# Kernel tuning notes

Hardware: AMD Instinct MI355X
Metric: run time of the kernel (lower is better)

## Reference

```python
import jax, jax.numpy as jnp
import numpy as np

EPS = 1e-12  # F.normalize eps

def _l2norm(t):
    n = jnp.linalg.norm(t, axis=-1, keepdims=True)
    return t / jnp.maximum(n, EPS)

def setup_inputs() -> dict:
    key = jax.random.key(0)
    ks = jax.random.split(key, 6)
    B, S, H, M = 4, 4096, 1024, 256
    x = jax.random.normal(ks[0], (B, S, H), dtype=jnp.float32)
    W_query = jax.random.normal(ks[1], (M, H), dtype=jnp.float32) * 0.02
    W_key = jax.random.normal(ks[2], (M, H), dtype=jnp.float32) * 0.02
    W_value = jax.random.normal(ks[3], (M, H), dtype=jnp.float32) * 0.02
    W_out = jax.random.normal(ks[4], (H, M), dtype=jnp.float32) * 0.02
    M0 = jnp.zeros((M, M), dtype=jnp.float32)
    return {"x": x, "W_query": W_query, "W_key": W_key, "W_value": W_value,
            "W_out": W_out, "M0": M0, "chunk_size": 64}

def reference(x, W_query, W_key, W_value, W_out, M0, chunk_size):
    B, S, H = x.shape
    Mdim = W_query.shape[0]
    decay, max_m_norm = 0.99, 10.0
    q = jnp.einsum('bsh,mh->bsm', x, W_query)
    k = _l2norm(jnp.einsum('bsh,mh->bsm', x, W_key))
    v = _l2norm(jnp.einsum('bsh,mh->bsm', x, W_value))
    n_chunks = S // chunk_size
    c = chunk_size
    # (n_chunks, B, c, Mdim) so scan iterates over chunks
    qc = q.reshape(B, n_chunks, c, Mdim).transpose(1, 0, 2, 3)
    kc = k.reshape(B, n_chunks, c, Mdim).transpose(1, 0, 2, 3)
    vc = v.reshape(B, n_chunks, c, Mdim).transpose(1, 0, 2, 3)

    def step(Mst, qkv):
        qch, kch, vch = qkv
        # read with state at start of chunk: q @ M.T
        r = jnp.einsum('bcm,nm->bcn', qch, Mst)
        # uniform write, token-level aggregation
        outer = jnp.einsum('bci,bcj->ij', vch, kch) / (B * c)
        Mn = decay * Mst + outer
        nrm = jnp.linalg.norm(Mn)
        Mn = Mn * (max_m_norm / jnp.maximum(nrm, max_m_norm))
        return Mn, r

    _, r_all = jax.lax.scan(step, M0, (qc, kc, vc))  # (n_chunks, B, c, Mdim)
    retrieved = r_all.transpose(1, 0, 2, 3).reshape(B, S, Mdim)
    out = jnp.einsum('bsm,hm->bsh', retrieved, W_out)
    return out
```

## Files before the change

kernel.cpp:

```cpp
#include <hip/hip_runtime.h>
#include <hip/hip_bf16.h>


typedef __attribute__((ext_vector_type(4))) float  f4;
typedef __attribute__((ext_vector_type(8))) short  bf16x8;

constexpr int   Hdim  = 1024;
constexpr int   Md    = 256;
constexpr float DECAY = 0.99f;
constexpr float MAXN  = 10.0f;

__device__ __forceinline__ unsigned short f2bf(float f) {
  union { float f; unsigned u; } v; v.f = f;
  unsigned r = v.u + 0x7FFFu + ((v.u >> 16) & 1u);
  return (unsigned short)(r >> 16);
}
__device__ __forceinline__ float bf2f(unsigned short h) {
  union { unsigned u; float f; } v; v.u = ((unsigned)h) << 16; return v.f;
}
__device__ __forceinline__ unsigned pk2bf(float a, float b) {
  __hip_bfloat162 h = __float22bfloat162_rn(make_float2(a, b));
  unsigned u; __builtin_memcpy(&u, &h, 4); return u;
}
__device__ __forceinline__ void gll16(const void* gptr, void* lptr) {
  __builtin_amdgcn_global_load_lds(
      (const __attribute__((address_space(1))) unsigned int*)gptr,
      (__attribute__((address_space(3))) unsigned int*)lptr, 16, 0, 0);
}

__global__ __launch_bounds__(256) void k0_wcvt(
    const float* __restrict__ Wq, const float* __restrict__ Wk,
    const float* __restrict__ Wv, const float* __restrict__ Wo,
    unsigned short* __restrict__ Wb, unsigned short* __restrict__ Wob,
    float* __restrict__ ssk, float* __restrict__ ssv)
{
  int gid = blockIdx.x * 256 + threadIdx.x;
  if (gid < 16384) ssk[gid] = 0.f;
  else if (gid < 32768) ssv[gid - 16384] = 0.f;
  const float* src; unsigned short* dst; int off;
  if (gid < 32768)      { src = Wq; dst = Wb;          off = gid; }
  else if (gid < 65536) { src = Wk; dst = Wb + 262144; off = gid - 32768; }
  else if (gid < 98304) { src = Wv; dst = Wb + 524288; off = gid - 65536; }
  else                  { src = Wo; dst = Wob;         off = gid - 98304; }
  float4 a = ((const float4*)src)[off * 2];
  float4 b = ((const float4*)src)[off * 2 + 1];
  ((uint4*)dst)[off] = make_uint4(pk2bf(a.x, a.y), pk2bf(a.z, a.w),
                                  pk2bf(b.x, b.y), pk2bf(b.z, b.w));
}

__global__ __launch_bounds__(256) void k1_proj(
    const float* __restrict__ x, const unsigned short* __restrict__ Wb,
    unsigned short* __restrict__ qp, unsigned short* __restrict__ kT,
    unsigned short* __restrict__ vT, float* __restrict__ ssk, float* __restrict__ ssv)
{
  __shared__ float          As[128 * 64];
  __shared__ unsigned short Bs[128 * 64];
  const int tid = threadIdx.x;
  const int g = blockIdx.x;
  const int xcd = g & 7, wq_ = g >> 3;
  const int ntile = wq_ % 6;
  const int strip = xcd * 16 + wq_ / 6;
  const int row0 = strip * 128;
  const int n0 = ntile * 128;
  const int seg = n0 >> 8;
  const int nw0 = n0 & 255;

  const int lane = tid & 63, wid = tid >> 6;
  const int wm = wid & 1, wn = wid >> 1;
  const int lr = lane & 15, lq = lane >> 4;
  const int arow_l = lane >> 4, aseg_l = lane & 15;
  const int brow_l = lane >> 3, bseg_l = lane & 7;

  f4 acc[4][4];
#pragma unroll
  for (int i = 0; i < 4; ++i)
#pragma unroll
    for (int j = 0; j < 4; ++j) acc[i][j] = f4{0.f, 0.f, 0.f, 0.f};

  for (int kk = 0; kk < Hdim; kk += 64) {
#pragma unroll
    for (int i = 0; i < 8; ++i) {
      int r = wid * 32 + i * 4 + arow_l;
      int s = aseg_l ^ (r & 15);
      gll16(&x[(long)(row0 + r) * Hdim + kk + s * 4], &As[(wid * 32 + i * 4) * 64]);
    }
#pragma unroll
    for (int i = 0; i < 4; ++i) {
      int r = wid * 32 + i * 8 + brow_l;
      int s = bseg_l ^ (r & 7);
      gll16(&Wb[(long)(n0 + r) * Hdim + kk + s * 8], &Bs[(wid * 32 + i * 8) * 64]);
    }
    __syncthreads();
#pragma unroll
    for (int ks = 0; ks < 2; ++ks) {
      bf16x8 af[4], bfr[4];
#pragma unroll
      for (int i = 0; i < 4; ++i) {
        int m = wm * 64 + i * 16 + lr;
        int p0 = (ks * 8 + lq * 2) ^ (m & 15);
        int p1 = p0 ^ 1;
        f4 a0 = *(const f4*)&As[m * 64 + p0 * 4];
        f4 a1 = *(const f4*)&As[m * 64 + p1 * 4];
        union { bf16x8 v; unsigned u[4]; } au;
        au.u[0] = pk2bf(a0[0], a0[1]); au.u[1] = pk2bf(a0[2], a0[3]);
        au.u[2] = pk2bf(a1[0], a1[1]); au.u[3] = pk2bf(a1[2], a1[3]);
        af[i] = au.v;
      }
#pragma unroll
      for (int j = 0; j < 4; ++j) {
        int n = wn * 64 + j * 16 + lr;
        int pb = (ks * 4 + lq) ^ (n & 7);
        bfr[j] = *(const bf16x8*)&Bs[n * 64 + pb * 8];
      }
#pragma unroll
      for (int i = 0; i < 4; ++i)
#pragma unroll
        for (int j = 0; j < 4; ++j)
          acc[i][j] = __builtin_amdgcn_mfma_f32_16x16x32_bf16(af[i], bfr[j], acc[i][j], 0, 0, 0);
    }
    __syncthreads();
  }

  if (seg == 0) {
#pragma unroll
    for (int i = 0; i < 4; ++i)
#pragma unroll
      for (int rr = 0; rr < 4; ++rr) {
        int token = row0 + wm * 64 + i * 16 + lq * 4 + rr;
        int b = token >> 12, s = token & 4095;
        int pidx = (s >> 6) * 256 + b * 64 + (s & 63);
#pragma unroll
        for (int j = 0; j < 4; ++j) {
          int nn = nw0 + wn * 64 + j * 16 + lr;
          qp[(long)pidx * Md + nn] = f2bf(acc[i][j][rr]);
        }
      }
  } else {
    unsigned short* dT = (seg == 1) ? kT : vT;
    float* ss = (seg == 1) ? ssk : ssv;
#pragma unroll
    for (int i = 0; i < 4; ++i)
#pragma unroll
      for (int rr = 0; rr < 4; ++rr) {
        int token = row0 + wm * 64 + i * 16 + lq * 4 + rr;
        int b = token >> 12, s = token & 4095;
        int pidx = (s >> 6) * 256 + b * 64 + (s & 63);
        int tch = pidx >> 8, tin = pidx & 255;
        float sq = 0.f;
#pragma unroll
        for (int j = 0; j < 4; ++j) {
          int nn = nw0 + wn * 64 + j * 16 + lr;
          float vv = acc[i][j][rr];
          dT[(long)tch * 65536 + nn * 256 + tin] = f2bf(vv);
          sq += vv * vv;
        }
        sq += __shfl_xor(sq, 1); sq += __shfl_xor(sq, 2);
        sq += __shfl_xor(sq, 4); sq += __shfl_xor(sq, 8);
        if (lr == 0) atomicAdd(&ss[pidx], sq);
      }
  }
}

__global__ __launch_bounds__(256) void k3_outer(
    const unsigned short* __restrict__ kT, const unsigned short* __restrict__ vT,
    const float* __restrict__ ssk, const float* __restrict__ ssv,
    float* __restrict__ O)
{
  __shared__ unsigned short As[64 * 64];
  __shared__ unsigned short Bs[256 * 64];
  __shared__ float sLs[256];
  const int tid = threadIdx.x;
  const int t = blockIdx.y;
  const int i0 = blockIdx.x * 64;
  const int lane = tid & 63, wid = tid >> 6;
  const int lr = lane & 15, lq = lane >> 4;
  const int drow = lane >> 3, dseg = lane & 7;

  {
    float a = ssv[t * 256 + tid], b = ssk[t * 256 + tid];
    sLs[tid] = rsqrtf(fmaxf(a, 1e-24f)) * rsqrtf(fmaxf(b, 1e-24f));
  }

  f4 acc[16];
#pragma unroll
  for (int q = 0; q < 16; ++q) acc[q] = f4{0.f, 0.f, 0.f, 0.f};

  for (int tok0 = 0; tok0 < 256; tok0 += 64) {
#pragma unroll
    for (int j = 0; j < 2; ++j) {
      int r = wid * 16 + j * 8 + drow;
      int s = dseg ^ (r & 7);
      gll16(&vT[(long)t * 65536 + (i0 + r) * 256 + tok0 + s * 8],
            &As[(wid * 16 + j * 8) * 64]);
    }
#pragma unroll
    for (int j = 0; j < 8; ++j) {
      int r = wid * 64 + j * 8 + drow;
      int s = dseg ^ (r & 7);
      gll16(&kT[(long)t * 65536 + r * 256 + tok0 + s * 8],
            &Bs[(wid * 64 + j * 8) * 64]);
    }
    __syncthreads();
#pragma unroll
    for (int ks = 0; ks < 2; ++ks) {
      int m = wid * 16 + lr;
      int pa = (ks * 4 + lq) ^ (m & 7);
      bf16x8 ar = *(const bf16x8*)&As[m * 64 + pa * 8];
      f4 s0 = *(const f4*)&sLs[tok0 + ks * 32 + lq * 8];
      f4 s1 = *(const f4*)&sLs[tok0 + ks * 32 + lq * 8 + 4];
      union { bf16x8 v; unsigned short e[8]; unsigned u[4]; } au;
      au.v = ar;
      au.u[0] = pk2bf(bf2f(au.e[0]) * s0[0], bf2f(au.e[1]) * s0[1]);
      au.u[1] = pk2bf(bf2f(au.e[2]) * s0[2], bf2f(au.e[3]) * s0[3]);
      au.u[2] = pk2bf(bf2f(au.e[4]) * s1[0], bf2f(au.e[5]) * s1[1]);
      au.u[3] = pk2bf(bf2f(au.e[6]) * s1[2], bf2f(au.e[7]) * s1[3]);
      bf16x8 af = au.v;
#pragma unroll
      for (int jf = 0; jf < 16; ++jf) {
        int n = jf * 16 + lr;
        int pb = (ks * 4 + lq) ^ (n & 7);
        bf16x8 bfr = *(const bf16x8*)&Bs[n * 64 + pb * 8];
        acc[jf] = __builtin_amdgcn_mfma_f32_16x16x32_bf16(af, bfr, acc[jf], 0, 0, 0);
      }
    }
    __syncthreads();
  }
  float* Ot = O + (long)t * 65536;
#pragma unroll
  for (int jf = 0; jf < 16; ++jf)
#pragma unroll
    for (int rr = 0; rr < 4; ++rr) {
      int i = i0 + wid * 16 + lq * 4 + rr;
      Ot[i * 256 + jf * 16 + lr] = acc[jf][rr] * (1.0f / 256.0f);
    }
}

__global__ __launch_bounds__(256) void k4_gram(const float* __restrict__ O, float* __restrict__ D)
{
  __shared__ unsigned short Tls[64][40];
  const int tid = threadIdx.x;
  const int kbase = blockIdx.x * 128;
  const int lane = tid & 63, wid = tid >> 6;
  const int lr = lane & 15, lq = lane >> 4;
  f4 acc[4];
#pragma unroll
  for (int q = 0; q < 4; ++q) acc[q] = f4{0.f, 0.f, 0.f, 0.f};

  for (int kk = 0; kk < 128; kk += 32) {
    int tk = tid & 7, tr = tid >> 3;
#pragma unroll
    for (int p = 0; p < 2; ++p) {
      int row = tr + 32 * p;
      float4 v = *(const float4*)&O[(long)row * 65536 + kbase + kk + tk * 4];
      *(uint2*)&Tls[row][tk * 4] = make_uint2(pk2bf(v.x, v.y), pk2bf(v.z, v.w));
    }
    __syncthreads();
    bf16x8 af = *(const bf16x8*)&Tls[wid * 16 + lr][lq * 8];
#pragma unroll
    for (int nt = 0; nt < 4; ++nt) {
      bf16x8 bfr = *(const bf16x8*)&Tls[nt * 16 + lr][lq * 8];
      acc[nt] = __builtin_amdgcn_mfma_f32_16x16x32_bf16(af, bfr, acc[nt], 0, 0, 0);
    }
    __syncthreads();
  }
#pragma unroll
  for (int nt = 0; nt < 4; ++nt)
#pragma unroll
    for (int rr = 0; rr < 4; ++rr)
      atomicAdd(&D[(wid * 16 + lq * 4 + rr) * 64 + nt * 16 + lr], acc[nt][rr]);
}

__global__ __launch_bounds__(256) void k56_mstate(const float* __restrict__ O,
    const float* __restrict__ D, unsigned short* __restrict__ Mb)
{
  __shared__ float Dl[64 * 65];
  __shared__ float sarr[64];
  const int tid = threadIdx.x;
  const int col = blockIdx.x * 256 + tid;
  float ov[64];
#pragma unroll
  for (int j = 0; j < 64; ++j) ov[j] = O[(long)j * 65536 + col];
  for (int i = tid; i < 4096; i += 256) Dl[(i >> 6) * 65 + (i & 63)] = D[i];
  __syncthreads();
  if (tid < 64) {
    const int lane = tid;
    float w = 0.f, nm2 = 0.f;
    for (int t = 0; t < 64; ++t) {
      float wt   = __shfl(w, t);
      float Dtt  = Dl[t * 65 + t];
      float nmn2 = DECAY * DECAY * nm2 + 2.f * DECAY * wt + Dtt;
      float nrm  = sqrtf(fmaxf(nmn2, 0.f));
      float s    = MAXN / fmaxf(nrm, MAXN);
      if (lane == 0) sarr[t] = s;
      w   = s * (DECAY * w + Dl[t * 65 + lane]);
      nm2 = s * s * nmn2;
    }
  }
  __syncthreads();
  float m = 0.f;
#pragma unroll
  for (int t = 0; t < 64; ++t) {
    Mb[(long)t * 65536 + col] = f2bf(m);
    m = sarr[t] * (DECAY * m + ov[t]);
  }
}

__global__ __launch_bounds__(256) void k7_rgemm(
    const unsigned short* __restrict__ qp, const unsigned short* __restrict__ Mb,
    unsigned short* __restrict__ rb)
{
  __shared__ unsigned short As[128 * 64];
  __shared__ unsigned short Bs[128 * 64];
  const int tid = threadIdx.x;
  const int t = blockIdx.z;
  const int row0 = t * 256 + blockIdx.y * 128;
  const int n0 = blockIdx.x * 128;
  const unsigned short* Bsrc = Mb + (long)t * 65536;
  const int lane = tid & 63, wid = tid >> 6;
  const int wm = wid & 1, wn = wid >> 1;
  const int lr = lane & 15, lq = lane >> 4;
  const int brow_l = lane >> 3, bseg_l = lane & 7;

  f4 acc[4][4];
#pragma unroll
  for (int i = 0; i < 4; ++i)
#pragma unroll
    for (int j = 0; j < 4; ++j) acc[i][j] = f4{0.f, 0.f, 0.f, 0.f};

  for (int kk = 0; kk < Md; kk += 64) {
#pragma unroll
    for (int i = 0; i < 4; ++i) {
      int r = wid * 32 + i * 8 + brow_l;
      int s = bseg_l ^ (r & 7);
      gll16(&qp[(long)(row0 + r) * Md + kk + s * 8], &As[(wid * 32 + i * 8) * 64]);
      gll16(&Bsrc[(long)(n0 + r) * Md + kk + s * 8], &Bs[(wid * 32 + i * 8) * 64]);
    }
    __syncthreads();
#pragma unroll
    for (int ks = 0; ks < 2; ++ks) {
      bf16x8 af[4], bfr[4];
#pragma unroll
      for (int i = 0; i < 4; ++i) {
        int m = wm * 64 + i * 16 + lr;
        int pa = (ks * 4 + lq) ^ (m & 7);
        af[i] = *(const bf16x8*)&As[m * 64 + pa * 8];
      }
#pragma unroll
      for (int j = 0; j < 4; ++j) {
        int n = wn * 64 + j * 16 + lr;
        int pb = (ks * 4 + lq) ^ (n & 7);
        bfr[j] = *(const bf16x8*)&Bs[n * 64 + pb * 8];
      }
#pragma unroll
      for (int i = 0; i < 4; ++i)
#pragma unroll
        for (int j = 0; j < 4; ++j)
          acc[i][j] = __builtin_amdgcn_mfma_f32_16x16x32_bf16(af[i], bfr[j], acc[i][j], 0, 0, 0);
    }
    __syncthreads();
  }
#pragma unroll
  for (int i = 0; i < 4; ++i)
#pragma unroll
    for (int rr = 0; rr < 4; ++rr) {
      int prow = row0 + wm * 64 + i * 16 + lq * 4 + rr;
#pragma unroll
      for (int j = 0; j < 4; ++j) {
        int n = n0 + wn * 64 + j * 16 + lr;
        rb[(long)prow * Md + n] = f2bf(acc[i][j][rr]);
      }
    }
}

__global__ __launch_bounds__(256) void k8_out(
    const unsigned short* __restrict__ rb, const unsigned short* __restrict__ Wob,
    float* __restrict__ out)
{
  __shared__ unsigned short As[128 * 64];
  __shared__ unsigned short Bs[128 * 64];
  const int tid = threadIdx.x;
  const int g = blockIdx.x;
  const int xcd = g & 7, wq_ = g >> 3;
  const int ntile = wq_ & 7;
  const int strip = xcd * 16 + (wq_ >> 3);
  const int n0 = ntile * 128;
  const int row0 = strip * 128;
  const int lane = tid & 63, wid = tid >> 6;
  const int wm = wid & 1, wn = wid >> 1;
  const int lr = lane & 15, lq = lane >> 4;
  const int brow_l = lane >> 3, bseg_l = lane & 7;

  f4 acc[4][4];
#pragma unroll
  for (int i = 0; i < 4; ++i)
#pragma unroll
    for (int j = 0; j < 4; ++j) acc[i][j] = f4{0.f, 0.f, 0.f, 0.f};

  for (int kk = 0; kk < Md; kk += 64) {
#pragma unroll
    for (int i = 0; i < 4; ++i) {
      int r = wid * 32 + i * 8 + brow_l;
      int s = bseg_l ^ (r & 7);
      gll16(&rb[(long)(row0 + r) * Md + kk + s * 8], &As[(wid * 32 + i * 8) * 64]);
      gll16(&Wob[(long)(n0 + r) * Md + kk + s * 8], &Bs[(wid * 32 + i * 8) * 64]);
    }
    __syncthreads();
#pragma unroll
    for (int ks = 0; ks < 2; ++ks) {
      bf16x8 af[4], bfr[4];
#pragma unroll
      for (int i = 0; i < 4; ++i) {
        int m = wm * 64 + i * 16 + lr;
        int pa = (ks * 4 + lq) ^ (m & 7);
        af[i] = *(const bf16x8*)&As[m * 64 + pa * 8];
      }
#pragma unroll
      for (int j = 0; j < 4; ++j) {
        int n = wn * 64 + j * 16 + lr;
        int pb = (ks * 4 + lq) ^ (n & 7);
        bfr[j] = *(const bf16x8*)&Bs[n * 64 + pb * 8];
      }
#pragma unroll
      for (int i = 0; i < 4; ++i)
#pragma unroll
        for (int j = 0; j < 4; ++j)
          acc[i][j] = __builtin_amdgcn_mfma_f32_16x16x32_bf16(af[i], bfr[j], acc[i][j], 0, 0, 0);
    }
    __syncthreads();
  }
#pragma unroll
  for (int i = 0; i < 4; ++i)
#pragma unroll
    for (int rr = 0; rr < 4; ++rr) {
      int pidx = row0 + wm * 64 + i * 16 + lq * 4 + rr;
      int t = pidx >> 8, rm = pidx & 255;
      int token = (rm >> 6) * 4096 + t * 64 + (rm & 63);
#pragma unroll
      for (int j = 0; j < 4; ++j) {
        int h = n0 + wn * 64 + j * 16 + lr;
        out[(long)token * Hdim + h] = acc[i][j][rr];
      }
    }
}

extern "C" void kernel_launch(void* const* d_in, const int* in_sizes, int n_in,
                              void* d_out, int out_size, void* d_ws, size_t ws_size,
                              hipStream_t stream) {
  (void)in_sizes; (void)n_in; (void)out_size; (void)ws_size;
  const float* x  = (const float*)d_in[0];
  const float* Wq = (const float*)d_in[1];
  const float* Wk = (const float*)d_in[2];
  const float* Wv = (const float*)d_in[3];
  const float* Wo = (const float*)d_in[4];
  float* out = (float*)d_out;
  char* ws = (char*)d_ws;

  unsigned short* qp  = (unsigned short*)(ws + 0);
  unsigned short* kT  = (unsigned short*)(ws + 8388608);
  unsigned short* vT  = (unsigned short*)(ws + 16777216);
  float* O    = (float*)(ws + 25165824);
  float* D    = (float*)(ws + 41943040);
  float* ssk  = (float*)(ws + 41959424);
  float* ssv  = (float*)(ws + 42024960);
  unsigned short* Wb  = (unsigned short*)(ws + 42090496);
  unsigned short* Wob = (unsigned short*)(ws + 43663360);
  unsigned short* Mb = vT;
  unsigned short* rb = kT;

  hipMemsetAsync(D, 0, 64 * 64 * sizeof(float), stream);
  k0_wcvt  <<<512,            256, 0, stream>>>(Wq, Wk, Wv, Wo, Wb, Wob, ssk, ssv);
  k1_proj  <<<768,            256, 0, stream>>>(x, Wb, qp, kT, vT, ssk, ssv);
  k3_outer <<<dim3(4, 64),    256, 0, stream>>>(kT, vT, ssk, ssv, O);
  k4_gram  <<<512,            256, 0, stream>>>(O, D);
  k56_mstate<<<256,           256, 0, stream>>>(O, D, Mb);
  k7_rgemm <<<dim3(2, 2, 64), 256, 0, stream>>>(qp, Mb, rb);
  k8_out   <<<1024,           256, 0, stream>>>(rb, Wob, out);
}
```

Baseline: 256.6 us.

## Split K/V transpose and norm reduction out of projection epilogue into separate kernel

The projection GEMM now writes k and v in row-major token layout like q, dropping the strided transposed stores and the per-row atomicAdd of squared norms. A new transpose kernel reads k and v rows, computes the squared norms without atomics, and writes the transposed layout through LDS with 16-byte stores. This targets the uncoalesced 2-byte scattered stores and atomic traffic in the GEMM epilogue. In exchange it adds an extra kernel launch and an additional round trip of 16 MB through memory, and the workspace layout is reshuffled so that O aliases the kb buffer.

```diff
diff --git a/kernel.cpp b/kernel.cpp
--- a/kernel.cpp
+++ b/kernel.cpp
@@ -31,12 +31,9 @@
 __global__ __launch_bounds__(256) void k0_wcvt(
     const float* __restrict__ Wq, const float* __restrict__ Wk,
     const float* __restrict__ Wv, const float* __restrict__ Wo,
-    unsigned short* __restrict__ Wb, unsigned short* __restrict__ Wob,
-    float* __restrict__ ssk, float* __restrict__ ssv)
+    unsigned short* __restrict__ Wb, unsigned short* __restrict__ Wob)
 {
   int gid = blockIdx.x * 256 + threadIdx.x;
-  if (gid < 16384) ssk[gid] = 0.f;
-  else if (gid < 32768) ssv[gid - 16384] = 0.f;
   const float* src; unsigned short* dst; int off;
   if (gid < 32768)      { src = Wq; dst = Wb;          off = gid; }
   else if (gid < 65536) { src = Wk; dst = Wb + 262144; off = gid - 32768; }
@@ -50,8 +47,8 @@
 
 __global__ __launch_bounds__(256) void k1_proj(
     const float* __restrict__ x, const unsigned short* __restrict__ Wb,
-    unsigned short* __restrict__ qp, unsigned short* __restrict__ kT,
-    unsigned short* __restrict__ vT, float* __restrict__ ssk, float* __restrict__ ssv)
+    unsigned short* __restrict__ qp, unsigned short* __restrict__ kb,
+    unsigned short* __restrict__ vb)
 {
   __shared__ float          As[128 * 64];
   __shared__ unsigned short Bs[128 * 64];
@@ -64,6 +61,7 @@
   const int n0 = ntile * 128;
   const int seg = n0 >> 8;
   const int nw0 = n0 & 255;
+  unsigned short* dst = (seg == 0) ? qp : ((seg == 1) ? kb : vb);
 
   const int lane = tid & 63, wid = tid >> 6;
   const int wm = wid & 1, wn = wid >> 1;
@@ -120,44 +118,65 @@
     }
     __syncthreads();
   }
-
-  if (seg == 0) {
-#pragma unroll
-    for (int i = 0; i < 4; ++i)
-#pragma unroll
-      for (int rr = 0; rr < 4; ++rr) {
-        int token = row0 + wm * 64 + i * 16 + lq * 4 + rr;
-        int b = token >> 12, s = token & 4095;
-        int pidx = (s >> 6) * 256 + b * 64 + (s & 63);
-#pragma unroll
-        for (int j = 0; j < 4; ++j) {
-          int nn = nw0 + wn * 64 + j * 16 + lr;
-          qp[(long)pidx * Md + nn] = f2bf(acc[i][j][rr]);
-        }
-      }
-  } else {
-    unsigned short* dT = (seg == 1) ? kT : vT;
-    float* ss = (seg == 1) ? ssk : ssv;
-#pragma unroll
-    for (int i = 0; i < 4; ++i)
-#pragma unroll
-      for (int rr = 0; rr < 4; ++rr) {
-        int token = row0 + wm * 64 + i * 16 + lq * 4 + rr;
-        int b = token >> 12, s = token & 4095;
-        int pidx = (s >> 6) * 256 + b * 64 + (s & 63);
-        int tch = pidx >> 8, tin = pidx & 255;
-        float sq = 0.f;
-#pragma unroll
-        for (int j = 0; j < 4; ++j) {
-          int nn = nw0 + wn * 64 + j * 16 + lr;
-          float vv = acc[i][j][rr];
-          dT[(long)tch * 65536 + nn * 256 + tin] = f2bf(vv);
-          sq += vv * vv;
-        }
-        sq += __shfl_xor(sq, 1); sq += __shfl_xor(sq, 2);
-        sq += __shfl_xor(sq, 4); sq += __shfl_xor(sq, 8);
-        if (lr == 0) atomicAdd(&ss[pidx], sq);
-      }
+#pragma unroll
+  for (int i = 0; i < 4; ++i)
+#pragma unroll
+    for (int rr = 0; rr < 4; ++rr) {
+      int token = row0 + wm * 64 + i * 16 + lq * 4 + rr;
+      int b = token >> 12, s = token & 4095;
+      int pidx = (s >> 6) * 256 + b * 64 + (s & 63);
+#pragma unroll
+      for (int j = 0; j < 4; ++j) {
+        int nn = nw0 + wn * 64 + j * 16 + lr;
+        dst[(long)pidx * Md + nn] = f2bf(acc[i][j][rr]);
+      }
+    }
+}
+
+__global__ __launch_bounds__(256) void k2_trans(
+    const unsigned short* __restrict__ kb, const unsigned short* __restrict__ vb,
+    unsigned short* __restrict__ kT, unsigned short* __restrict__ vT,
+    float* __restrict__ ssk, float* __restrict__ ssv)
+{
+  __shared__ unsigned short Tls[256 * 68];
+  __shared__ float red[256];
+  const int tid = threadIdx.x;
+  const int g = blockIdx.x;
+  const int t = g >> 2, a = (g >> 1) & 1, h = g & 1;
+  const unsigned short* src = a ? vb : kb;
+  unsigned short* dst = a ? vT : kT;
+  float* ss = a ? ssv : ssk;
+  const int w = tid >> 6, l = tid & 63;
+  const int ms = tid >> 3, seg = tid & 7;
+#pragma unroll
+  for (int sub = 0; sub < 2; ++sub) {
+    const int tin0 = h * 128 + sub * 64;
+    const unsigned short* row = src + ((long)t * 256 + tin0 + l) * 256 + w * 64;
+    float sq = 0.f;
+#pragma unroll
+    for (int i = 0; i < 16; ++i) {
+      ushort4 vv = *(const ushort4*)&row[i * 4];
+      float f0 = bf2f(vv.x), f1 = bf2f(vv.y), f2 = bf2f(vv.z), f3 = bf2f(vv.w);
+      sq += f0 * f0 + f1 * f1 + f2 * f2 + f3 * f3;
+      int m = w * 64 + i * 4;
+      Tls[(m + 0) * 68 + l] = vv.x;
+      Tls[(m + 1) * 68 + l] = vv.y;
+      Tls[(m + 2) * 68 + l] = vv.z;
+      Tls[(m + 3) * 68 + l] = vv.w;
+    }
+    red[tid] = sq;
+    __syncthreads();
+    if (tid < 64)
+      ss[t * 256 + tin0 + tid] = red[tid] + red[64 + tid] + red[128 + tid] + red[192 + tid];
+    unsigned short* drow = dst + (long)t * 65536 + tin0 + seg * 8;
+#pragma unroll
+    for (int k = 0; k < 8; ++k) {
+      int m = k * 32 + ms;
+      uint2 lo = *(const uint2*)&Tls[m * 68 + seg * 8];
+      uint2 hi = *(const uint2*)&Tls[m * 68 + seg * 8 + 4];
+      *(uint4*)&drow[(long)m * 256] = make_uint4(lo.x, lo.y, hi.x, hi.y);
+    }
+    __syncthreads();
   }
 }
 
@@ -456,23 +475,26 @@
   char* ws = (char*)d_ws;
 
   unsigned short* qp  = (unsigned short*)(ws + 0);
-  unsigned short* kT  = (unsigned short*)(ws + 8388608);
-  unsigned short* vT  = (unsigned short*)(ws + 16777216);
-  float* O    = (float*)(ws + 25165824);
+  unsigned short* kb  = (unsigned short*)(ws + 8388608);
+  unsigned short* vb  = (unsigned short*)(ws + 16777216);
+  unsigned short* kT  = (unsigned short*)(ws + 25165824);
+  unsigned short* vT  = (unsigned short*)(ws + 33554432);
+  float* O    = (float*)(ws + 8388608);
   float* D    = (float*)(ws + 41943040);
   float* ssk  = (float*)(ws + 41959424);
   float* ssv  = (float*)(ws + 42024960);
   unsigned short* Wb  = (unsigned short*)(ws + 42090496);
   unsigned short* Wob = (unsigned short*)(ws + 43663360);
+  unsigned short* rb = kT;
   unsigned short* Mb = vT;
-  unsigned short* rb = kT;
 
   hipMemsetAsync(D, 0, 64 * 64 * sizeof(float), stream);
-  k0_wcvt  <<<512,            256, 0, stream>>>(Wq, Wk, Wv, Wo, Wb, Wob, ssk, ssv);
-  k1_proj  <<<768,            256, 0, stream>>>(x, Wb, qp, kT, vT, ssk, ssv);
-  k3_outer <<<dim3(4, 64),    256, 0, stream>>>(kT, vT, ssk, ssv, O);
-  k4_gram  <<<512,            256, 0, stream>>>(O, D);
-  k56_mstate<<<256,           256, 0, stream>>>(O, D, Mb);
-  k7_rgemm <<<dim3(2, 2, 64), 256, 0, stream>>>(qp, Mb, rb);
-  k8_out   <<<1024,           256, 0, stream>>>(rb, Wob, out);
-}
+  k0_wcvt   <<<512,            256, 0, stream>>>(Wq, Wk, Wv, Wo, Wb, Wob);
+  k1_proj   <<<768,            256, 0, stream>>>(x, Wb, qp, kb, vb);
+  k2_trans  <<<256,            256, 0, stream>>>(kb, vb, kT, vT, ssk, ssv);
+  k3_outer  <<<dim3(4, 64),    256, 0, stream>>>(kT, vT, ssk, ssv, O);
+  k4_gram   <<<512,            256, 0, stream>>>(O, D);
+  k56_mstate<<<256,            256, 0, stream>>>(O, D, Mb);
+  k7_rgemm  <<<dim3(2, 2, 64), 256, 0, stream>>>(qp, Mb, rb);
+  k8_out    <<<1024,           256, 0, stream>>>(rb, Wob, out);
+}
```

Result: faster. 231.0 us (-10.0%).
